# Performance work log

Measured on AMD Instinct MI355X. Metric: run time of the kernel, lower is better.

Reference implementation:

```python
import jax, jax.numpy as jnp
import numpy as np

NUM_USERS = 1_000_000
NUM_ITEMS = 500_000
NUM_GENRES = 20
NUM_TAGS = 100
EMBEDDING_DIM = 64
HIDDEN_UNITS = [256, 128, 64]
NUM_CLASSES = 5
BATCH = 16384


def setup_inputs() -> dict:
    key = jax.random.key(0)
    ks = jax.random.split(key, 16)
    deep_in = EMBEDDING_DIM * 2 + NUM_GENRES + NUM_TAGS  # 248
    inp = {
        "user": jax.random.randint(ks[0], (BATCH,), 0, NUM_USERS),
        "item": jax.random.randint(ks[1], (BATCH,), 0, NUM_ITEMS),
        "genre": jax.random.uniform(ks[2], (BATCH, NUM_GENRES), dtype=jnp.float32),
        "tag": jax.random.uniform(ks[3], (BATCH, NUM_TAGS), dtype=jnp.float32),
        # wide Linear(num_users+num_items -> HIDDEN_UNITS[-1]); stored transposed
        # as (vocab, out) so the one-hot matmul becomes a row gather.
        "wide_W": jax.random.normal(ks[4], (NUM_USERS + NUM_ITEMS, HIDDEN_UNITS[-1]), dtype=jnp.float32) * 0.01,
        "wide_b": jnp.zeros((HIDDEN_UNITS[-1],), dtype=jnp.float32),
        "user_emb": jax.random.normal(ks[5], (NUM_USERS, EMBEDDING_DIM), dtype=jnp.float32) * 0.01,
        "item_emb": jax.random.normal(ks[6], (NUM_ITEMS, EMBEDDING_DIM), dtype=jnp.float32) * 0.01,
        "W0": jax.random.normal(ks[7], (deep_in, HIDDEN_UNITS[0]), dtype=jnp.float32) * 0.02,
        "b0": jnp.zeros((HIDDEN_UNITS[0],), dtype=jnp.float32),
        "W1": jax.random.normal(ks[8], (HIDDEN_UNITS[0], HIDDEN_UNITS[1]), dtype=jnp.float32) * 0.02,
        "b1": jnp.zeros((HIDDEN_UNITS[1],), dtype=jnp.float32),
        "W2": jax.random.normal(ks[9], (HIDDEN_UNITS[1], HIDDEN_UNITS[2]), dtype=jnp.float32) * 0.02,
        "b2": jnp.zeros((HIDDEN_UNITS[2],), dtype=jnp.float32),
        "final_W": jax.random.normal(ks[10], (HIDDEN_UNITS[-1] * 2, NUM_CLASSES), dtype=jnp.float32) * 0.02,
        "final_b": jnp.zeros((NUM_CLASSES,), dtype=jnp.float32),
    }
    return inp


def reference(user, item, genre, tag, wide_W, wide_b, user_emb, item_emb,
              W0, b0, W1, b1, W2, b2, final_W, final_b):
    # Wide path: one_hot(user)++one_hot(item) @ W + b  ==  gather+sum of rows.
    wide_out = wide_W[user] + wide_W[NUM_USERS + item] + wide_b  # [B, 64]
    # Deep path (dropout is identity in eval mode).
    u = user_emb[user]   # [B, E]
    v = item_emb[item]   # [B, E]
    h = jnp.concatenate([u, v, genre, tag], axis=1)  # [B, 248]
    h = jax.nn.relu(h @ W0 + b0)
    h = jax.nn.relu(h @ W1 + b1)
    h = jax.nn.relu(h @ W2 + b2)  # [B, 64]
    combined = jnp.concatenate([h, wide_out], axis=1)  # [B, 128]
    logits = combined @ final_W + final_b  # [B, NUM_CLASSES]
    return logits
```

## Files before the change

kernel.cpp:

```cpp
#include <hip/hip_runtime.h>

#define BATCH 16384
#define NU 1000000
#define TBR 64
#define MT 512
#define WSOFF0 0
#define WSOFF1 65536
#define WSOFF2 98304
#define WSREQ  212992

typedef __attribute__((ext_vector_type(8))) short short8;
typedef __attribute__((ext_vector_type(4))) short short4v;
typedef __attribute__((ext_vector_type(4))) float f32x4;

__device__ __forceinline__ unsigned short f32_bf16(float f) {
    unsigned int u = __float_as_uint(f);
    u += 0x7FFF + ((u >> 16) & 1);
    return (unsigned short)(u >> 16);
}
__device__ __forceinline__ float bf16_f32(unsigned short h) {
    return __uint_as_float(((unsigned int)h) << 16);
}

__device__ __forceinline__ int swz(int row, int byteInRow, int rowStrideB) {
    return row * rowStrideB + (byteInRow ^ ((row & 7) << 4));
}

__device__ __forceinline__ short8 cvt8(float4 a, float4 b) {
    short8 s;
    s[0] = (short)f32_bf16(a.x); s[1] = (short)f32_bf16(a.y);
    s[2] = (short)f32_bf16(a.z); s[3] = (short)f32_bf16(a.w);
    s[4] = (short)f32_bf16(b.x); s[5] = (short)f32_bf16(b.y);
    s[6] = (short)f32_bf16(b.z); s[7] = (short)f32_bf16(b.w);
    return s;
}

__global__ void prep_weights(const float* __restrict__ W0, const float* __restrict__ W1,
                             const float* __restrict__ W2, unsigned short* __restrict__ ws)
{
    __shared__ float t[64 * 65];
    int b = blockIdx.x;
    const float* src; unsigned short* dst; int K, N, K2, k0, n0;
    if (b < 16)      { src = W0; dst = ws + WSOFF0; K = 248; N = 256; K2 = 256; k0 = (b >> 2) * 64; n0 = (b & 3) * 64; }
    else if (b < 24) { int i = b - 16; src = W1; dst = ws + WSOFF1; K = 256; N = 128; K2 = 256; k0 = (i >> 1) * 64; n0 = (i & 1) * 64; }
    else             { int i = b - 24; src = W2; dst = ws + WSOFF2; K = 128; N = 64;  K2 = 128; k0 = i * 64; n0 = 0; }

    int tid = threadIdx.x;
    for (int q = tid; q < 64 * 16; q += 256) {
        int k = q >> 4, nq = q & 15;
        float4 v = make_float4(0.f, 0.f, 0.f, 0.f);
        if (k0 + k < K) v = *(const float4*)(src + (size_t)(k0 + k) * N + n0 + nq * 4);
        t[k * 65 + nq * 4 + 0] = v.x;
        t[k * 65 + nq * 4 + 1] = v.y;
        t[k * 65 + nq * 4 + 2] = v.z;
        t[k * 65 + nq * 4 + 3] = v.w;
    }
    __syncthreads();
    for (int q = tid; q < 64 * 8; q += 256) {
        int n = q >> 3, kg = q & 7;
        short8 o;
        #pragma unroll
        for (int i = 0; i < 8; ++i) o[i] = (short)f32_bf16(t[(kg * 8 + i) * 65 + n]);
        *(short8*)(dst + (size_t)(n0 + n) * K2 + k0 + kg * 8) = o;
    }
}

__global__ __launch_bounds__(MT, 1) void wd_mfma(
        const int* __restrict__ user, const int* __restrict__ item,
        const float* __restrict__ genre, const float* __restrict__ tag,
        const float* __restrict__ wide_W, const float* __restrict__ wide_b,
        const float* __restrict__ user_emb, const float* __restrict__ item_emb,
        const float* __restrict__ b0, const float* __restrict__ b1,
        const float* __restrict__ b2,
        const float* __restrict__ fW, const float* __restrict__ fb,
        const unsigned short* __restrict__ ws, float* __restrict__ out)
{
    __shared__ unsigned short sX[TBR * 256];
    __shared__ unsigned short sH0[TBR * 256];
    __shared__ unsigned short sH1[TBR * 128];
    __shared__ unsigned short sH2[TBR * 72];
    __shared__ unsigned short sWide[TBR * 72];
    __shared__ float sFW[640];

    const int tid = threadIdx.x;
    const int row0 = blockIdx.x * TBR;
    const unsigned short* w0t = ws + WSOFF0;
    const unsigned short* w1t = ws + WSOFF1;
    const unsigned short* w2t = ws + WSOFF2;

    const int wid = tid >> 6;
    const int lane = tid & 63;
    const int lr = lane & 15;
    const int lh = lane >> 4;

    const int cb0 = wid * 32;
    const int cb1 = wid * 16;
    short8 B0[2][8];
    #pragma unroll
    for (int t = 0; t < 2; ++t)
        #pragma unroll
        for (int kc = 0; kc < 8; ++kc)
            B0[t][kc] = *(const short8*)(w0t + (size_t)(cb0 + t * 16 + lr) * 256 + kc * 32 + lh * 8);
    short8 B1[8];
    #pragma unroll
    for (int kc = 0; kc < 8; ++kc)
        B1[kc] = *(const short8*)(w1t + (size_t)(cb1 + lr) * 256 + kc * 32 + lh * 8);
    float rb0[2];
    rb0[0] = b0[cb0 + lr]; rb0[1] = b0[cb0 + 16 + lr];
    float rb1 = b1[cb1 + lr];
    float rb2 = b2[(wid & 3) * 16 + lr];

    #pragma unroll
    for (int it = 0; it < 6; ++it) {
        int q = tid + it * MT;
        if (it < 4) {
            int r = q >> 5, j = q & 31;
            int grow = row0 + r;
            float4 va = make_float4(0.f, 0.f, 0.f, 0.f);
            float4 vb = va;
            if (j < 8) {
                const float4* p = (const float4*)(user_emb + (size_t)user[grow] * 64);
                va = p[j * 2]; vb = p[j * 2 + 1];
            } else if (j < 16) {
                const float4* p = (const float4*)(item_emb + (size_t)item[grow] * 64);
                va = p[(j - 8) * 2]; vb = p[(j - 8) * 2 + 1];
            } else if (j == 16) {
                const float4* p = (const float4*)(genre + (size_t)grow * 20);
                va = p[0]; vb = p[1];
            } else if (j == 17) {
                const float4* p = (const float4*)(genre + (size_t)grow * 20);
                va = p[2]; vb = p[3];
            } else if (j == 18) {
                va = *(const float4*)(genre + (size_t)grow * 20 + 16);
                vb = *(const float4*)(tag + (size_t)grow * 100);
            } else if (j < 31) {
                const float4* p = (const float4*)(tag + (size_t)grow * 100 + 4);
                int jj = j - 19;
                va = p[jj * 2]; vb = p[jj * 2 + 1];
            }
            *(short8*)((char*)sX + swz(r, j * 16, 512)) = cvt8(va, vb);
        } else {
            int p = q - 4 * MT;
            int r = p >> 4, j = p & 15;
            int grow = row0 + r;
            float4 a = ((const float4*)(wide_W + (size_t)user[grow] * 64))[j];
            float4 b = ((const float4*)(wide_W + (size_t)(NU + item[grow]) * 64))[j];
            float4 c = ((const float4*)wide_b)[j];
            short4v o;
            o[0] = (short)f32_bf16(a.x + b.x + c.x);
            o[1] = (short)f32_bf16(a.y + b.y + c.y);
            o[2] = (short)f32_bf16(a.z + b.z + c.z);
            o[3] = (short)f32_bf16(a.w + b.w + c.w);
            *(short4v*)(sWide + r * 72 + j * 4) = o;
        }
    }
    if (tid < 160) {
        ((float4*)sFW)[tid] = ((const float4*)fW)[tid];
    }
    __syncthreads();

    {
        f32x4 acc[4][2];
        #pragma unroll
        for (int rt = 0; rt < 4; ++rt)
            #pragma unroll
            for (int t = 0; t < 2; ++t) acc[rt][t] = (f32x4)(0.f);

        #pragma unroll
        for (int kc = 0; kc < 8; ++kc) {
            const int kb = kc * 32 + lh * 8;
            short8 a[4];
            #pragma unroll
            for (int rt = 0; rt < 4; ++rt)
                a[rt] = *(const short8*)((const char*)sX + swz(rt * 16 + lr, kb * 2, 512));
            #pragma unroll
            for (int t = 0; t < 2; ++t)
                #pragma unroll
                for (int rt = 0; rt < 4; ++rt)
                    acc[rt][t] = __builtin_amdgcn_mfma_f32_16x16x32_bf16(a[rt], B0[t][kc], acc[rt][t], 0, 0, 0);
        }
        #pragma unroll
        for (int t = 0; t < 2; ++t) {
            #pragma unroll
            for (int rt = 0; rt < 4; ++rt)
                #pragma unroll
                for (int jj = 0; jj < 4; ++jj) {
                    int row = rt * 16 + lh * 4 + jj;
                    float v = fmaxf(acc[rt][t][jj] + rb0[t], 0.f);
                    *(unsigned short*)((char*)sH0 + swz(row, (cb0 + t * 16 + lr) * 2, 512)) = f32_bf16(v);
                }
        }
        __syncthreads();
    }

    {
        f32x4 acc[4];
        #pragma unroll
        for (int rt = 0; rt < 4; ++rt) acc[rt] = (f32x4)(0.f);

        #pragma unroll
        for (int kc = 0; kc < 8; ++kc) {
            const int kb = kc * 32 + lh * 8;
            short8 a[4];
            #pragma unroll
            for (int rt = 0; rt < 4; ++rt)
                a[rt] = *(const short8*)((const char*)sH0 + swz(rt * 16 + lr, kb * 2, 512));
            #pragma unroll
            for (int rt = 0; rt < 4; ++rt)
                acc[rt] = __builtin_amdgcn_mfma_f32_16x16x32_bf16(a[rt], B1[kc], acc[rt], 0, 0, 0);
        }
        #pragma unroll
        for (int rt = 0; rt < 4; ++rt)
            #pragma unroll
            for (int jj = 0; jj < 4; ++jj) {
                int row = rt * 16 + lh * 4 + jj;
                float v = fmaxf(acc[rt][jj] + rb1, 0.f);
                *(unsigned short*)((char*)sH1 + swz(row, (cb1 + lr) * 2, 256)) = f32_bf16(v);
            }
        __syncthreads();
    }

    {
        const int t = wid & 3;
        const int rtb = (wid >> 2) * 2;
        const int cbase = t * 16;
        f32x4 acc[2];
        acc[0] = (f32x4)(0.f); acc[1] = (f32x4)(0.f);

        #pragma unroll
        for (int kc = 0; kc < 4; ++kc) {
            const int kb = kc * 32 + lh * 8;
            short8 bf = *(const short8*)(w2t + (size_t)(cbase + lr) * 128 + kb);
            #pragma unroll
            for (int rr = 0; rr < 2; ++rr) {
                short8 a = *(const short8*)((const char*)sH1 + swz((rtb + rr) * 16 + lr, kb * 2, 256));
                acc[rr] = __builtin_amdgcn_mfma_f32_16x16x32_bf16(a, bf, acc[rr], 0, 0, 0);
            }
        }
        #pragma unroll
        for (int rr = 0; rr < 2; ++rr)
            #pragma unroll
            for (int jj = 0; jj < 4; ++jj) {
                int row = (rtb + rr) * 16 + lh * 4 + jj;
                sH2[row * 72 + cbase + lr] = f32_bf16(fmaxf(acc[rr][jj] + rb2, 0.f));
            }
        __syncthreads();
    }

    if (tid < TBR * 5) {
        int r = tid / 5, c = tid - r * 5;
        float acc = fb[c];
        #pragma unroll
        for (int kq = 0; kq < 8; ++kq) {
            short8 h = *(const short8*)(sH2 + r * 72 + kq * 8);
            #pragma unroll
            for (int i = 0; i < 8; ++i)
                acc = fmaf(bf16_f32((unsigned short)h[i]), sFW[(kq * 8 + i) * 5 + c], acc);
        }
        #pragma unroll
        for (int kq = 0; kq < 8; ++kq) {
            short8 h = *(const short8*)(sWide + r * 72 + kq * 8);
            #pragma unroll
            for (int i = 0; i < 8; ++i)
                acc = fmaf(bf16_f32((unsigned short)h[i]), sFW[(64 + kq * 8 + i) * 5 + c], acc);
        }
        out[(size_t)(row0 + r) * 5 + c] = acc;
    }
}

#define NTHR 256
#define TB 32

__device__ __forceinline__ void fma4(float4& a, float s, const float4& w) {
    a.x = fmaf(s, w.x, a.x); a.y = fmaf(s, w.y, a.y);
    a.z = fmaf(s, w.z, a.z); a.w = fmaf(s, w.w, a.w);
}
__device__ __forceinline__ float4 add4(const float4& a, const float4& b) {
    return make_float4(a.x + b.x, a.y + b.y, a.z + b.z, a.w + b.w);
}
__device__ __forceinline__ float4 relu4(const float4& a) {
    return make_float4(fmaxf(a.x, 0.f), fmaxf(a.y, 0.f), fmaxf(a.z, 0.f), fmaxf(a.w, 0.f));
}

__global__ void wd_fused(const int* __restrict__ user, const int* __restrict__ item,
                         const float* __restrict__ genre, const float* __restrict__ tag,
                         const float* __restrict__ wide_W, const float* __restrict__ wide_b,
                         const float* __restrict__ user_emb, const float* __restrict__ item_emb,
                         const float* __restrict__ W0, const float* __restrict__ b0,
                         const float* __restrict__ W1, const float* __restrict__ b1,
                         const float* __restrict__ W2, const float* __restrict__ b2,
                         const float* __restrict__ fW, const float* __restrict__ fb,
                         float* __restrict__ out)
{
    __shared__ float sA[TB * 248];
    __shared__ float sB[TB * 256];
    __shared__ float sC[TB * 64];

    const int tid = threadIdx.x;
    const int row0 = blockIdx.x * TB;

    for (int q = tid; q < TB * 62; q += NTHR) {
        int r = q / 62, j = q - r * 62, grow = row0 + r;
        float4 v;
        if (j < 16) v = reinterpret_cast<const float4*>(user_emb + (size_t)user[grow] * 64)[j];
        else if (j < 32) v = reinterpret_cast<const float4*>(item_emb + (size_t)item[grow] * 64)[j - 16];
        else if (j < 37) v = reinterpret_cast<const float4*>(genre + (size_t)grow * 20)[j - 32];
        else v = reinterpret_cast<const float4*>(tag + (size_t)grow * 100)[j - 37];
        *reinterpret_cast<float4*>(sA + r * 248 + j * 4) = v;
    }
    for (int q = tid; q < TB * 16; q += NTHR) {
        int r = q >> 4, j = q & 15, grow = row0 + r;
        float4 a = reinterpret_cast<const float4*>(wide_W + (size_t)user[grow] * 64)[j];
        float4 b = reinterpret_cast<const float4*>(wide_W + (size_t)(NU + item[grow]) * 64)[j];
        float4 c = reinterpret_cast<const float4*>(wide_b)[j];
        *reinterpret_cast<float4*>(sC + r * 64 + j * 4) =
            make_float4(a.x + b.x + c.x, a.y + b.y + c.y, a.z + b.z + c.z, a.w + b.w + c.w);
    }
    __syncthreads();
    {
        const int cg = tid & 63, r0 = (tid >> 6) * 8;
        float4 acc[8];
        #pragma unroll
        for (int r = 0; r < 8; ++r) acc[r] = make_float4(0.f, 0.f, 0.f, 0.f);
        for (int k = 0; k < 248; k += 4) {
            const float4* wp = reinterpret_cast<const float4*>(W0 + (size_t)k * 256) + cg;
            float4 w0 = wp[0], w1 = wp[64], w2 = wp[128], w3 = wp[192];
            #pragma unroll
            for (int r = 0; r < 8; ++r) {
                float4 xv = *reinterpret_cast<const float4*>(sA + (r0 + r) * 248 + k);
                fma4(acc[r], xv.x, w0); fma4(acc[r], xv.y, w1);
                fma4(acc[r], xv.z, w2); fma4(acc[r], xv.w, w3);
            }
        }
        float4 bb = reinterpret_cast<const float4*>(b0)[cg];
        #pragma unroll
        for (int r = 0; r < 8; ++r)
            *reinterpret_cast<float4*>(sB + (r0 + r) * 256 + cg * 4) = relu4(add4(acc[r], bb));
    }
    __syncthreads();
    {
        const int cg = tid & 31, r0 = (tid >> 5) * 4;
        float4 acc[4];
        #pragma unroll
        for (int r = 0; r < 4; ++r) acc[r] = make_float4(0.f, 0.f, 0.f, 0.f);
        for (int k = 0; k < 256; k += 4) {
            const float4* wp = reinterpret_cast<const float4*>(W1 + (size_t)k * 128) + cg;
            float4 w0 = wp[0], w1 = wp[32], w2 = wp[64], w3 = wp[96];
            #pragma unroll
            for (int r = 0; r < 4; ++r) {
                float4 xv = *reinterpret_cast<const float4*>(sB + (r0 + r) * 256 + k);
                fma4(acc[r], xv.x, w0); fma4(acc[r], xv.y, w1);
                fma4(acc[r], xv.z, w2); fma4(acc[r], xv.w, w3);
            }
        }
        float4 bb = reinterpret_cast<const float4*>(b1)[cg];
        #pragma unroll
        for (int r = 0; r < 4; ++r)
            *reinterpret_cast<float4*>(sA + (r0 + r) * 128 + cg * 4) = relu4(add4(acc[r], bb));
    }
    __syncthreads();
    {
        const int cg = tid & 15, r0 = (tid >> 4) * 2;
        float4 acc[2];
        acc[0] = make_float4(0.f, 0.f, 0.f, 0.f); acc[1] = acc[0];
        for (int k = 0; k < 128; k += 4) {
            const float4* wp = reinterpret_cast<const float4*>(W2 + (size_t)k * 64) + cg;
            float4 w0 = wp[0], w1 = wp[16], w2 = wp[32], w3 = wp[48];
            #pragma unroll
            for (int r = 0; r < 2; ++r) {
                float4 xv = *reinterpret_cast<const float4*>(sA + (r0 + r) * 128 + k);
                fma4(acc[r], xv.x, w0); fma4(acc[r], xv.y, w1);
                fma4(acc[r], xv.z, w2); fma4(acc[r], xv.w, w3);
            }
        }
        float4 bb = reinterpret_cast<const float4*>(b2)[cg];
        #pragma unroll
        for (int r = 0; r < 2; ++r)
            *reinterpret_cast<float4*>(sB + (r0 + r) * 64 + cg * 4) = relu4(add4(acc[r], bb));
    }
    __syncthreads();
    if (tid < TB * 5) {
        int r = tid / 5, c = tid - r * 5;
        float acc = fb[c];
        for (int k = 0; k < 64; ++k) acc = fmaf(sB[r * 64 + k], fW[k * 5 + c], acc);
        for (int k = 0; k < 64; ++k) acc = fmaf(sC[r * 64 + k], fW[(64 + k) * 5 + c], acc);
        out[(size_t)(row0 + r) * 5 + c] = acc;
    }
}

extern "C" void kernel_launch(void* const* d_in, const int* in_sizes, int n_in,
                              void* d_out, int out_size, void* d_ws, size_t ws_size,
                              hipStream_t stream) {
    const int* user = (const int*)d_in[0];
    const int* item = (const int*)d_in[1];
    const float* genre = (const float*)d_in[2];
    const float* tag = (const float*)d_in[3];
    const float* wide_W = (const float*)d_in[4];
    const float* wide_b = (const float*)d_in[5];
    const float* user_emb = (const float*)d_in[6];
    const float* item_emb = (const float*)d_in[7];
    const float* W0 = (const float*)d_in[8];
    const float* b0 = (const float*)d_in[9];
    const float* W1 = (const float*)d_in[10];
    const float* b1 = (const float*)d_in[11];
    const float* W2 = (const float*)d_in[12];
    const float* b2 = (const float*)d_in[13];
    const float* fW = (const float*)d_in[14];
    const float* fb = (const float*)d_in[15];
    float* out = (float*)d_out;

    if (ws_size >= (size_t)WSREQ) {
        hipLaunchKernelGGL(prep_weights, dim3(26), dim3(256), 0, stream,
                           W0, W1, W2, (unsigned short*)d_ws);
        hipLaunchKernelGGL(wd_mfma, dim3(BATCH / TBR), dim3(MT), 0, stream,
                           user, item, genre, tag, wide_W, wide_b, user_emb, item_emb,
                           b0, b1, b2, fW, fb, (const unsigned short*)d_ws, out);
    } else {
        hipLaunchKernelGGL(wd_fused, dim3(BATCH / TB), dim3(NTHR), 0, stream,
                           user, item, genre, tag, wide_W, wide_b, user_emb, item_emb,
                           W0, b0, W1, b1, W2, b2, fW, fb, out);
    }
}
```

Baseline: 30.87 us.

## Drop weight-prep kernel; build bf16 MFMA fragments directly from fp32 weights

Removes the separate prep_weights launch that transposed and converted W0/W1/W2 into a bf16 workspace. Each wave now builds its B-fragments by strided fp32 loads from the original weights and converts them in registers, and W2 fragments are also preloaded. Global gathers for embeddings and the wide path are hoisted into registers before the weight loads so their latency overlaps. This saves a kernel launch and a dependency, but every one of the 256 blocks now does scalar, uncoalesced strided weight reads and conversions, and register pressure goes up.

```diff
diff --git a/kernel.cpp b/kernel.cpp
--- a/kernel.cpp
+++ b/kernel.cpp
@@ -4,10 +4,6 @@
 #define NU 1000000
 #define TBR 64
 #define MT 512
-#define WSOFF0 0
-#define WSOFF1 65536
-#define WSOFF2 98304
-#define WSREQ  212992
 
 typedef __attribute__((ext_vector_type(8))) short short8;
 typedef __attribute__((ext_vector_type(4))) short short4v;
@@ -35,34 +31,16 @@
     return s;
 }
 
-__global__ void prep_weights(const float* __restrict__ W0, const float* __restrict__ W1,
-                             const float* __restrict__ W2, unsigned short* __restrict__ ws)
-{
-    __shared__ float t[64 * 65];
-    int b = blockIdx.x;
-    const float* src; unsigned short* dst; int K, N, K2, k0, n0;
-    if (b < 16)      { src = W0; dst = ws + WSOFF0; K = 248; N = 256; K2 = 256; k0 = (b >> 2) * 64; n0 = (b & 3) * 64; }
-    else if (b < 24) { int i = b - 16; src = W1; dst = ws + WSOFF1; K = 256; N = 128; K2 = 256; k0 = (i >> 1) * 64; n0 = (i & 1) * 64; }
-    else             { int i = b - 24; src = W2; dst = ws + WSOFF2; K = 128; N = 64;  K2 = 128; k0 = i * 64; n0 = 0; }
-
-    int tid = threadIdx.x;
-    for (int q = tid; q < 64 * 16; q += 256) {
-        int k = q >> 4, nq = q & 15;
-        float4 v = make_float4(0.f, 0.f, 0.f, 0.f);
-        if (k0 + k < K) v = *(const float4*)(src + (size_t)(k0 + k) * N + n0 + nq * 4);
-        t[k * 65 + nq * 4 + 0] = v.x;
-        t[k * 65 + nq * 4 + 1] = v.y;
-        t[k * 65 + nq * 4 + 2] = v.z;
-        t[k * 65 + nq * 4 + 3] = v.w;
-    }
-    __syncthreads();
-    for (int q = tid; q < 64 * 8; q += 256) {
-        int n = q >> 3, kg = q & 7;
-        short8 o;
-        #pragma unroll
-        for (int i = 0; i < 8; ++i) o[i] = (short)f32_bf16(t[(kg * 8 + i) * 65 + n]);
-        *(short8*)(dst + (size_t)(n0 + n) * K2 + k0 + kg * 8) = o;
-    }
+__device__ __forceinline__ short8 mk_frag(const float* __restrict__ W, int N, int K,
+                                          int col, int kb) {
+    short8 f;
+    #pragma unroll
+    for (int i = 0; i < 8; ++i) {
+        int k = kb + i;
+        float v = (k < K) ? W[(size_t)k * N + col] : 0.f;
+        f[i] = (short)f32_bf16(v);
+    }
+    return f;
 }
 
 __global__ __launch_bounds__(MT, 1) void wd_mfma(
@@ -70,10 +48,11 @@
         const float* __restrict__ genre, const float* __restrict__ tag,
         const float* __restrict__ wide_W, const float* __restrict__ wide_b,
         const float* __restrict__ user_emb, const float* __restrict__ item_emb,
-        const float* __restrict__ b0, const float* __restrict__ b1,
-        const float* __restrict__ b2,
+        const float* __restrict__ W0, const float* __restrict__ b0,
+        const float* __restrict__ W1, const float* __restrict__ b1,
+        const float* __restrict__ W2, const float* __restrict__ b2,
         const float* __restrict__ fW, const float* __restrict__ fb,
-        const unsigned short* __restrict__ ws, float* __restrict__ out)
+        float* __restrict__ out)
 {
     __shared__ unsigned short sX[TBR * 256];
     __shared__ unsigned short sH0[TBR * 256];
@@ -84,79 +63,99 @@
 
     const int tid = threadIdx.x;
     const int row0 = blockIdx.x * TBR;
-    const unsigned short* w0t = ws + WSOFF0;
-    const unsigned short* w1t = ws + WSOFF1;
-    const unsigned short* w2t = ws + WSOFF2;
 
     const int wid = tid >> 6;
     const int lane = tid & 63;
     const int lr = lane & 15;
     const int lh = lane >> 4;
 
+    float4 xa[4], xb[4];
+    #pragma unroll
+    for (int it = 0; it < 4; ++it) {
+        int q = tid + it * MT;
+        int r = q >> 5, j = q & 31;
+        int grow = row0 + r;
+        float4 va = make_float4(0.f, 0.f, 0.f, 0.f);
+        float4 vb = va;
+        if (j < 8) {
+            const float4* p = (const float4*)(user_emb + (size_t)user[grow] * 64);
+            va = p[j * 2]; vb = p[j * 2 + 1];
+        } else if (j < 16) {
+            const float4* p = (const float4*)(item_emb + (size_t)item[grow] * 64);
+            va = p[(j - 8) * 2]; vb = p[(j - 8) * 2 + 1];
+        } else if (j == 16) {
+            const float4* p = (const float4*)(genre + (size_t)grow * 20);
+            va = p[0]; vb = p[1];
+        } else if (j == 17) {
+            const float4* p = (const float4*)(genre + (size_t)grow * 20);
+            va = p[2]; vb = p[3];
+        } else if (j == 18) {
+            va = *(const float4*)(genre + (size_t)grow * 20 + 16);
+            vb = *(const float4*)(tag + (size_t)grow * 100);
+        } else if (j < 31) {
+            const float4* p = (const float4*)(tag + (size_t)grow * 100 + 4);
+            int jj = j - 19;
+            va = p[jj * 2]; vb = p[jj * 2 + 1];
+        }
+        xa[it] = va; xb[it] = vb;
+    }
+    float4 wa[2], wb[2];
+    {
+        int j = tid & 15;
+        #pragma unroll
+        for (int it = 0; it < 2; ++it) {
+            int q = tid + it * MT;
+            int r = q >> 4;
+            int grow = row0 + r;
+            wa[it] = ((const float4*)(wide_W + (size_t)user[grow] * 64))[j];
+            wb[it] = ((const float4*)(wide_W + (size_t)(NU + item[grow]) * 64))[j];
+        }
+    }
+    float4 wc = ((const float4*)wide_b)[tid & 15];
+    float4 fwv = make_float4(0.f, 0.f, 0.f, 0.f);
+    if (tid < 160) fwv = ((const float4*)fW)[tid];
+
     const int cb0 = wid * 32;
     const int cb1 = wid * 16;
+    const int cb2 = (wid & 3) * 16;
     short8 B0[2][8];
     #pragma unroll
     for (int t = 0; t < 2; ++t)
         #pragma unroll
         for (int kc = 0; kc < 8; ++kc)
-            B0[t][kc] = *(const short8*)(w0t + (size_t)(cb0 + t * 16 + lr) * 256 + kc * 32 + lh * 8);
+            B0[t][kc] = mk_frag(W0, 256, 248, cb0 + t * 16 + lr, kc * 32 + lh * 8);
     short8 B1[8];
     #pragma unroll
     for (int kc = 0; kc < 8; ++kc)
-        B1[kc] = *(const short8*)(w1t + (size_t)(cb1 + lr) * 256 + kc * 32 + lh * 8);
+        B1[kc] = mk_frag(W1, 128, 256, cb1 + lr, kc * 32 + lh * 8);
+    short8 B2f[4];
+    #pragma unroll
+    for (int kc = 0; kc < 4; ++kc)
+        B2f[kc] = mk_frag(W2, 64, 128, cb2 + lr, kc * 32 + lh * 8);
+
     float rb0[2];
     rb0[0] = b0[cb0 + lr]; rb0[1] = b0[cb0 + 16 + lr];
     float rb1 = b1[cb1 + lr];
-    float rb2 = b2[(wid & 3) * 16 + lr];
-
-    #pragma unroll
-    for (int it = 0; it < 6; ++it) {
+    float rb2 = b2[cb2 + lr];
+
+    #pragma unroll
+    for (int it = 0; it < 4; ++it) {
         int q = tid + it * MT;
-        if (it < 4) {
-            int r = q >> 5, j = q & 31;
-            int grow = row0 + r;
-            float4 va = make_float4(0.f, 0.f, 0.f, 0.f);
-            float4 vb = va;
-            if (j < 8) {
-                const float4* p = (const float4*)(user_emb + (size_t)user[grow] * 64);
-                va = p[j * 2]; vb = p[j * 2 + 1];
-            } else if (j < 16) {
-                const float4* p = (const float4*)(item_emb + (size_t)item[grow] * 64);
-                va = p[(j - 8) * 2]; vb = p[(j - 8) * 2 + 1];
-            } else if (j == 16) {
-                const float4* p = (const float4*)(genre + (size_t)grow * 20);
-                va = p[0]; vb = p[1];
-            } else if (j == 17) {
-                const float4* p = (const float4*)(genre + (size_t)grow * 20);
-                va = p[2]; vb = p[3];
-            } else if (j == 18) {
-                va = *(const float4*)(genre + (size_t)grow * 20 + 16);
-                vb = *(const float4*)(tag + (size_t)grow * 100);
-            } else if (j < 31) {
-                const float4* p = (const float4*)(tag + (size_t)grow * 100 + 4);
-                int jj = j - 19;
-                va = p[jj * 2]; vb = p[jj * 2 + 1];
-            }
-            *(short8*)((char*)sX + swz(r, j * 16, 512)) = cvt8(va, vb);
-        } else {
-            int p = q - 4 * MT;
-            int r = p >> 4, j = p & 15;
-            int grow = row0 + r;
-            float4 a = ((const float4*)(wide_W + (size_t)user[grow] * 64))[j];
-            float4 b = ((const float4*)(wide_W + (size_t)(NU + item[grow]) * 64))[j];
-            float4 c = ((const float4*)wide_b)[j];
-            short4v o;
-            o[0] = (short)f32_bf16(a.x + b.x + c.x);
-            o[1] = (short)f32_bf16(a.y + b.y + c.y);
-            o[2] = (short)f32_bf16(a.z + b.z + c.z);
-            o[3] = (short)f32_bf16(a.w + b.w + c.w);
-            *(short4v*)(sWide + r * 72 + j * 4) = o;
-        }
-    }
-    if (tid < 160) {
-        ((float4*)sFW)[tid] = ((const float4*)fW)[tid];
-    }
+        int r = q >> 5, j = q & 31;
+        *(short8*)((char*)sX + swz(r, j * 16, 512)) = cvt8(xa[it], xb[it]);
+    }
+    #pragma unroll
+    for (int it = 0; it < 2; ++it) {
+        int q = tid + it * MT;
+        int r = q >> 4, j = q & 15;
+        short4v o;
+        o[0] = (short)f32_bf16(wa[it].x + wb[it].x + wc.x);
+        o[1] = (short)f32_bf16(wa[it].y + wb[it].y + wc.y);
+        o[2] = (short)f32_bf16(wa[it].z + wb[it].z + wc.z);
+        o[3] = (short)f32_bf16(wa[it].w + wb[it].w + wc.w);
+        *(short4v*)(sWide + r * 72 + j * 4) = o;
+    }
+    if (tid < 160) ((float4*)sFW)[tid] = fwv;
     __syncthreads();
 
     {
@@ -221,20 +220,17 @@
     }
 
     {
-        const int t = wid & 3;
         const int rtb = (wid >> 2) * 2;
-        const int cbase = t * 16;
         f32x4 acc[2];
         acc[0] = (f32x4)(0.f); acc[1] = (f32x4)(0.f);
 
         #pragma unroll
         for (int kc = 0; kc < 4; ++kc) {
             const int kb = kc * 32 + lh * 8;
-            short8 bf = *(const short8*)(w2t + (size_t)(cbase + lr) * 128 + kb);
             #pragma unroll
             for (int rr = 0; rr < 2; ++rr) {
                 short8 a = *(const short8*)((const char*)sH1 + swz((rtb + rr) * 16 + lr, kb * 2, 256));
-                acc[rr] = __builtin_amdgcn_mfma_f32_16x16x32_bf16(a, bf, acc[rr], 0, 0, 0);
+                acc[rr] = __builtin_amdgcn_mfma_f32_16x16x32_bf16(a, B2f[kc], acc[rr], 0, 0, 0);
             }
         }
         #pragma unroll
@@ -242,7 +238,7 @@
             #pragma unroll
             for (int jj = 0; jj < 4; ++jj) {
                 int row = (rtb + rr) * 16 + lh * 4 + jj;
-                sH2[row * 72 + cbase + lr] = f32_bf16(fmaxf(acc[rr][jj] + rb2, 0.f));
+                sH2[row * 72 + cb2 + lr] = f32_bf16(fmaxf(acc[rr][jj] + rb2, 0.f));
             }
         __syncthreads();
     }
@@ -264,126 +260,6 @@
             for (int i = 0; i < 8; ++i)
                 acc = fmaf(bf16_f32((unsigned short)h[i]), sFW[(64 + kq * 8 + i) * 5 + c], acc);
         }
-        out[(size_t)(row0 + r) * 5 + c] = acc;
-    }
-}
-
-#define NTHR 256
-#define TB 32
-
-__device__ __forceinline__ void fma4(float4& a, float s, const float4& w) {
-    a.x = fmaf(s, w.x, a.x); a.y = fmaf(s, w.y, a.y);
-    a.z = fmaf(s, w.z, a.z); a.w = fmaf(s, w.w, a.w);
-}
-__device__ __forceinline__ float4 add4(const float4& a, const float4& b) {
-    return make_float4(a.x + b.x, a.y + b.y, a.z + b.z, a.w + b.w);
-}
-__device__ __forceinline__ float4 relu4(const float4& a) {
-    return make_float4(fmaxf(a.x, 0.f), fmaxf(a.y, 0.f), fmaxf(a.z, 0.f), fmaxf(a.w, 0.f));
-}
-
-__global__ void wd_fused(const int* __restrict__ user, const int* __restrict__ item,
-                         const float* __restrict__ genre, const float* __restrict__ tag,
-                         const float* __restrict__ wide_W, const float* __restrict__ wide_b,
-                         const float* __restrict__ user_emb, const float* __restrict__ item_emb,
-                         const float* __restrict__ W0, const float* __restrict__ b0,
-                         const float* __restrict__ W1, const float* __restrict__ b1,
-                         const float* __restrict__ W2, const float* __restrict__ b2,
-                         const float* __restrict__ fW, const float* __restrict__ fb,
-                         float* __restrict__ out)
-{
-    __shared__ float sA[TB * 248];
-    __shared__ float sB[TB * 256];
-    __shared__ float sC[TB * 64];
-
-    const int tid = threadIdx.x;
-    const int row0 = blockIdx.x * TB;
-
-    for (int q = tid; q < TB * 62; q += NTHR) {
-        int r = q / 62, j = q - r * 62, grow = row0 + r;
-        float4 v;
-        if (j < 16) v = reinterpret_cast<const float4*>(user_emb + (size_t)user[grow] * 64)[j];
-        else if (j < 32) v = reinterpret_cast<const float4*>(item_emb + (size_t)item[grow] * 64)[j - 16];
-        else if (j < 37) v = reinterpret_cast<const float4*>(genre + (size_t)grow * 20)[j - 32];
-        else v = reinterpret_cast<const float4*>(tag + (size_t)grow * 100)[j - 37];
-        *reinterpret_cast<float4*>(sA + r * 248 + j * 4) = v;
-    }
-    for (int q = tid; q < TB * 16; q += NTHR) {
-        int r = q >> 4, j = q & 15, grow = row0 + r;
-        float4 a = reinterpret_cast<const float4*>(wide_W + (size_t)user[grow] * 64)[j];
-        float4 b = reinterpret_cast<const float4*>(wide_W + (size_t)(NU + item[grow]) * 64)[j];
-        float4 c = reinterpret_cast<const float4*>(wide_b)[j];
-        *reinterpret_cast<float4*>(sC + r * 64 + j * 4) =
-            make_float4(a.x + b.x + c.x, a.y + b.y + c.y, a.z + b.z + c.z, a.w + b.w + c.w);
-    }
-    __syncthreads();
-    {
-        const int cg = tid & 63, r0 = (tid >> 6) * 8;
-        float4 acc[8];
-        #pragma unroll
-        for (int r = 0; r < 8; ++r) acc[r] = make_float4(0.f, 0.f, 0.f, 0.f);
-        for (int k = 0; k < 248; k += 4) {
-            const float4* wp = reinterpret_cast<const float4*>(W0 + (size_t)k * 256) + cg;
-            float4 w0 = wp[0], w1 = wp[64], w2 = wp[128], w3 = wp[192];
-            #pragma unroll
-            for (int r = 0; r < 8; ++r) {
-                float4 xv = *reinterpret_cast<const float4*>(sA + (r0 + r) * 248 + k);
-                fma4(acc[r], xv.x, w0); fma4(acc[r], xv.y, w1);
-                fma4(acc[r], xv.z, w2); fma4(acc[r], xv.w, w3);
-            }
-        }
-        float4 bb = reinterpret_cast<const float4*>(b0)[cg];
-        #pragma unroll
-        for (int r = 0; r < 8; ++r)
-            *reinterpret_cast<float4*>(sB + (r0 + r) * 256 + cg * 4) = relu4(add4(acc[r], bb));
-    }
-    __syncthreads();
-    {
-        const int cg = tid & 31, r0 = (tid >> 5) * 4;
-        float4 acc[4];
-        #pragma unroll
-        for (int r = 0; r < 4; ++r) acc[r] = make_float4(0.f, 0.f, 0.f, 0.f);
-        for (int k = 0; k < 256; k += 4) {
-            const float4* wp = reinterpret_cast<const float4*>(W1 + (size_t)k * 128) + cg;
-            float4 w0 = wp[0], w1 = wp[32], w2 = wp[64], w3 = wp[96];
-            #pragma unroll
-            for (int r = 0; r < 4; ++r) {
-                float4 xv = *reinterpret_cast<const float4*>(sB + (r0 + r) * 256 + k);
-                fma4(acc[r], xv.x, w0); fma4(acc[r], xv.y, w1);
-                fma4(acc[r], xv.z, w2); fma4(acc[r], xv.w, w3);
-            }
-        }
-        float4 bb = reinterpret_cast<const float4*>(b1)[cg];
-        #pragma unroll
-        for (int r = 0; r < 4; ++r)
-            *reinterpret_cast<float4*>(sA + (r0 + r) * 128 + cg * 4) = relu4(add4(acc[r], bb));
-    }
-    __syncthreads();
-    {
-        const int cg = tid & 15, r0 = (tid >> 4) * 2;
-        float4 acc[2];
-        acc[0] = make_float4(0.f, 0.f, 0.f, 0.f); acc[1] = acc[0];
-        for (int k = 0; k < 128; k += 4) {
-            const float4* wp = reinterpret_cast<const float4*>(W2 + (size_t)k * 64) + cg;
-            float4 w0 = wp[0], w1 = wp[16], w2 = wp[32], w3 = wp[48];
-            #pragma unroll
-            for (int r = 0; r < 2; ++r) {
-                float4 xv = *reinterpret_cast<const float4*>(sA + (r0 + r) * 128 + k);
-                fma4(acc[r], xv.x, w0); fma4(acc[r], xv.y, w1);
-                fma4(acc[r], xv.z, w2); fma4(acc[r], xv.w, w3);
-            }
-        }
-        float4 bb = reinterpret_cast<const float4*>(b2)[cg];
-        #pragma unroll
-        for (int r = 0; r < 2; ++r)
-            *reinterpret_cast<float4*>(sB + (r0 + r) * 64 + cg * 4) = relu4(add4(acc[r], bb));
-    }
-    __syncthreads();
-    if (tid < TB * 5) {
-        int r = tid / 5, c = tid - r * 5;
-        float acc = fb[c];
-        for (int k = 0; k < 64; ++k) acc = fmaf(sB[r * 64 + k], fW[k * 5 + c], acc);
-        for (int k = 0; k < 64; ++k) acc = fmaf(sC[r * 64 + k], fW[(64 + k) * 5 + c], acc);
         out[(size_t)(row0 + r) * 5 + c] = acc;
     }
 }
@@ -409,15 +285,7 @@
     const float* fb = (const float*)d_in[15];
     float* out = (float*)d_out;
 
-    if (ws_size >= (size_t)WSREQ) {
-        hipLaunchKernelGGL(prep_weights, dim3(26), dim3(256), 0, stream,
-                           W0, W1, W2, (unsigned short*)d_ws);
-        hipLaunchKernelGGL(wd_mfma, dim3(BATCH / TBR), dim3(MT), 0, stream,
-                           user, item, genre, tag, wide_W, wide_b, user_emb, item_emb,
-                           b0, b1, b2, fW, fb, (const unsigned short*)d_ws, out);
-    } else {
-        hipLaunchKernelGGL(wd_fused, dim3(BATCH / TB), dim3(NTHR), 0, stream,
-                           user, item, genre, tag, wide_W, wide_b, user_emb, item_emb,
-                           W0, b0, W1, b1, W2, b2, fW, fb, out);
-    }
-}
+    hipLaunchKernelGGL(wd_mfma, dim3(BATCH / TBR), dim3(MT), 0, stream,
+                       user, item, genre, tag, wide_W, wide_b, user_emb, item_emb,
+                       W0, b0, W1, b1, W2, b2, fW, fb, out);
+}
```

Result: slower. 39.87 us (+29.2%).
